# Performance work log

Hardware: AMD Instinct MI355X
Metric: run time of the kernel (lower is better)

Reference implementation:

```python
import jax, jax.numpy as jnp
import numpy as np

DEPTH, HEADS, DIM_HEAD = 6, 8, 64
B, N, E = 2, 128, 160
NUM_ATOMS, NF = 100, 127
DIM = NF + 1                 # 128, node feature dim fed to transformer
INNER = HEADS * DIM_HEAD     # 512


def setup_inputs() -> dict:
    key = jax.random.key(0)
    ks = iter(jax.random.split(key, 40))
    f32 = jnp.float32
    def w(shape, scale=0.02):
        return jax.random.normal(next(ks), shape, dtype=f32) * scale
    inp = {
        "indices": jax.random.randint(next(ks), (B, N), 0, NUM_ATOMS),
        "coordinates": jax.random.normal(next(ks), (B, N, 3), dtype=f32),
        "bonds": jax.random.randint(next(ks), (E, 2), 0, N),
        "noise_level": jax.random.uniform(next(ks), (1,), dtype=f32),
        "atom_emb": w((NUM_ATOMS, NF), 1.0),
        "ln1_g": jnp.ones((DEPTH, DIM), f32), "ln1_b": jnp.zeros((DEPTH, DIM), f32),
        "Wq": w((DEPTH, DIM, INNER)), "bq": jnp.zeros((DEPTH, INNER), f32),
        "Wkv": w((DEPTH, DIM, 2 * INNER)), "bkv": jnp.zeros((DEPTH, 2 * INNER), f32),
        "We": w((DEPTH, 3, INNER)), "be": jnp.zeros((DEPTH, INNER), f32),
        "Wo": w((DEPTH, INNER, DIM)), "bo": jnp.zeros((DEPTH, DIM), f32),
        "Wg1": w((DEPTH, 3 * DIM, 1)),
        "ln2_g": jnp.ones((DEPTH, DIM), f32), "ln2_b": jnp.zeros((DEPTH, DIM), f32),
        "W1": w((DEPTH, DIM, 4 * DIM)), "b1": jnp.zeros((DEPTH, 4 * DIM), f32),
        "W2": w((DEPTH, 4 * DIM, DIM)), "b2": jnp.zeros((DEPTH, DIM), f32),
        "Wg2": w((DEPTH, 3 * DIM, 1)),
        "Wlin": w((DIM, 1)), "blin": jnp.zeros((1,), f32),
    }
    return inp


def _ln(x, g, b, eps=1e-5):
    m = jnp.mean(x, -1, keepdims=True)
    v = jnp.mean((x - m) ** 2, -1, keepdims=True)
    return (x - m) * jax.lax.rsqrt(v + eps) * g + b


def _gated_residual(x, res, Wg):
    # gate = sigmoid(Linear([x, res, x-res])); out = x*gate + res*(1-gate)
    gate = jax.nn.sigmoid(jnp.concatenate([x, res, x - res], -1) @ Wg)  # (B,N,1)
    return x * gate + res * (1.0 - gate)


def _forward(indices, bonds, coordinates, noise_level, atom_emb,
             ln1_g, ln1_b, Wq, bq, Wkv, bkv, We, be, Wo, bo, Wg1,
             ln2_g, ln2_b, W1, b1, W2, b2, Wg2, Wlin, blin):
    b, n = indices.shape
    # nodes_embedding: atom embedding + noise-level channel
    noise = jnp.broadcast_to(noise_level.reshape(1, 1, 1).astype(coordinates.dtype), (b, n, 1))
    nodes = jnp.concatenate([atom_emb[indices], noise], -1)  # (B,N,DIM)
    # edges_embedding: vectorized scatter of per-bond coordinate differences
    i, j = bonds[:, 0], bonds[:, 1]
    diff = coordinates[:, i] - coordinates[:, j]             # (B,E,3)
    edges = jnp.zeros((b, n, n, 3), coordinates.dtype)
    edges = edges.at[:, i, j].set(diff).at[:, j, i].set(-diff)

    scale = DIM_HEAD ** -0.5
    for l in range(DEPTH):
        # PreNorm + edge-biased attention (mask is all-ones -> no-op)
        xn = _ln(nodes, ln1_g[l], ln1_b[l])
        q = (xn @ Wq[l] + bq[l]).reshape(b, n, HEADS, DIM_HEAD)
        k, v = jnp.split(xn @ Wkv[l] + bkv[l], 2, -1)
        k = k.reshape(b, n, HEADS, DIM_HEAD)
        v = v.reshape(b, n, HEADS, DIM_HEAD)
        e = (edges @ We[l] + be[l]).reshape(b, n, n, HEADS, DIM_HEAD)
        kk = k[:, None] + e                                   # (B,i,j,H,D)
        vv = v[:, None] + e
        sim = jnp.einsum('bihd,bijhd->bijh', q, kk) * scale
        attn = jax.nn.softmax(sim, axis=2)                    # softmax over j
        out = jnp.einsum('bijh,bijhd->bihd', attn, vv).reshape(b, n, INNER)
        out = out @ Wo[l] + bo[l]
        nodes = _gated_residual(out, nodes, Wg1[l])
        # PreNorm + FeedForward (exact GELU, mult=4) + gated residual
        xn = _ln(nodes, ln2_g[l], ln2_b[l])
        ff = jax.nn.gelu(xn @ W1[l] + b1[l], approximate=False) @ W2[l] + b2[l]
        nodes = _gated_residual(ff, nodes, Wg2[l])
    return jnp.sum(nodes @ Wlin + blin)


def reference(indices, coordinates, bonds, noise_level, atom_emb,
              ln1_g, ln1_b, Wq, bq, Wkv, bkv, We, be, Wo, bo, Wg1,
              ln2_g, ln2_b, W1, b1, W2, b2, Wg2, Wlin, blin):
    return _forward(indices, bonds, coordinates, noise_level, atom_emb,
                    ln1_g, ln1_b, Wq, bq, Wkv, bkv, We, be, Wo, bo, Wg1,
                    ln2_g, ln2_b, W1, b1, W2, b2, Wg2, Wlin, blin)
```

## Files before the change

### kernel.cpp

```cpp
#include <hip/hip_runtime.h>
#include <hip/hip_fp16.h>
#include <math.h>

#define DEPTH 6
#define NN    128
#define EE    160
#define NF    127
#define DIMM  128
#define INNER 512
#define NNODE 256

typedef _Float16 h2f16 __attribute__((ext_vector_type(2)));

#if defined(__has_builtin)
#if __has_builtin(__builtin_amdgcn_fdot2)
#define HAVE_FDOT2 1
#endif
#endif

__device__ __forceinline__ float fdot2f(h2f16 a, h2f16 b, float c) {
#ifdef HAVE_FDOT2
    return __builtin_amdgcn_fdot2(a, b, c, false);
#else
    return c + (float)a.x * (float)b.x + (float)a.y * (float)b.y;
#endif
}

__device__ __forceinline__ void gload16(const void* g, void* l) {
    __builtin_amdgcn_global_load_lds((const __attribute__((address_space(1))) void*)g,
                                     (__attribute__((address_space(3))) void*)l,
                                     16, 0, 0);
}

template <int N>
__device__ __forceinline__ void wait_vm() {
    __builtin_amdgcn_s_waitcnt((0xF << 8) | (7 << 4) | (N & 0xF) | ((N >> 4) << 14));
}
__device__ __forceinline__ void wait_lgkm0() { __builtin_amdgcn_s_waitcnt(0xC07F); }
__device__ __forceinline__ void sbar0() { __builtin_amdgcn_sched_barrier(0); }

__device__ __forceinline__ void stage16(const char* g, char* lds, int ln) {
#pragma unroll
    for (int i = 0; i < 16; i++)
        gload16(g + i * 1024 + ln * 16, lds + i * 1024);
}


template <int NSTAGE>
__device__ __forceinline__ float gemv512T(const __half* s_xh, const float* wbuf,
                                          const char* nextG, char* wbufc, int ln) {
    const float4* W = (const float4*)((const char*)wbuf + ln * 256);
    const float4* X = (const float4*)s_xh;
    float acc = 0.0f;
    float4 wr[8], xr[8];
#pragma unroll
    for (int i = 0; i < 8; i++) { wr[i] = W[(i + ln) & 15]; xr[i] = X[i]; }
#pragma unroll
    for (int i = 0; i < 8; i++) {
        const h2f16* wh = (const h2f16*)&wr[i];
        const h2f16* xh = (const h2f16*)&xr[i];
        acc = fdot2f(xh[0], wh[0], acc); acc = fdot2f(xh[1], wh[1], acc);
        acc = fdot2f(xh[2], wh[2], acc); acc = fdot2f(xh[3], wh[3], acc);
    }
    float4 wr2[8], xr2[8];
#pragma unroll
    for (int i = 0; i < 8; i++) { wr2[i] = W[(i + 8 + ln) & 15]; xr2[i] = X[i + 8]; }
    if (NSTAGE) {
        sbar0();
        wait_lgkm0();
        sbar0();
        stage16(nextG, wbufc, ln);
    }
#pragma unroll
    for (int i = 0; i < 8; i++) {
        const h2f16* wh = (const h2f16*)&wr2[i];
        const h2f16* xh = (const h2f16*)&xr2[i];
        acc = fdot2f(xh[0], wh[0], acc); acc = fdot2f(xh[1], wh[1], acc);
        acc = fdot2f(xh[2], wh[2], acc); acc = fdot2f(xh[3], wh[3], acc);
    }
    return acc;
}

template <int NSTAGE>
__device__ __forceinline__ float gemv128T(const __half* s_xp, const float* wbuf,
                                          const char* nextG, char* wbufc, int ln) {
    int kq = ln & 3;
    const float4* W = (const float4*)((const char*)wbuf + ln * 256);
    const float4* X = (const float4*)((const char*)s_xp + kq * 272);
    float acc = 0.0f;
    float4 wr[8], xr[8];
#pragma unroll
    for (int i = 0; i < 8; i++) { wr[i] = W[(i + ln) & 15]; xr[i] = X[i]; }
#pragma unroll
    for (int i = 0; i < 8; i++) {
        const h2f16* wh = (const h2f16*)&wr[i];
        const h2f16* xh = (const h2f16*)&xr[i];
        acc = fdot2f(xh[0], wh[0], acc); acc = fdot2f(xh[1], wh[1], acc);
        acc = fdot2f(xh[2], wh[2], acc); acc = fdot2f(xh[3], wh[3], acc);
    }
    float4 wr2[8], xr2[8];
#pragma unroll
    for (int i = 0; i < 8; i++) { wr2[i] = W[(i + 8 + ln) & 15]; xr2[i] = X[i + 8]; }
    if (NSTAGE) {
        sbar0();
        wait_lgkm0();
        sbar0();
        stage16(nextG, wbufc, ln);
    }
#pragma unroll
    for (int i = 0; i < 8; i++) {
        const h2f16* wh = (const h2f16*)&wr2[i];
        const h2f16* xh = (const h2f16*)&xr2[i];
        acc = fdot2f(xh[0], wh[0], acc); acc = fdot2f(xh[1], wh[1], acc);
        acc = fdot2f(xh[2], wh[2], acc); acc = fdot2f(xh[3], wh[3], acc);
    }
    return acc;
}

template <int N>
__device__ __forceinline__ void block_reduce_n(float* vals, float* sbuf) {
#pragma unroll
    for (int off = 32; off > 0; off >>= 1)
#pragma unroll
        for (int q = 0; q < N; q++) vals[q] += __shfl_xor(vals[q], off, 64);
    int wave = threadIdx.x >> 6;
    if ((threadIdx.x & 63) == 0)
#pragma unroll
        for (int q = 0; q < N; q++) sbuf[wave * N + q] = vals[q];
    __syncthreads();
#pragma unroll
    for (int q = 0; q < N; q++) {
        float r = 0.0f;
#pragma unroll
        for (int g = 0; g < 8; g++) r += sbuf[g * N + q];
        vals[q] = r;
    }
    __syncthreads();
}

__device__ __forceinline__ float gelu_exact(float a) {
    return 0.5f * a * (1.0f + erff(a * 0.70710678f));
}

__global__ __launch_bounds__(512) void k_cvt(const float* Wq, const float* Wkv,
                                             const float* Wo, const float* W1,
                                             const float* W2,
                                             __half* hWq, __half* hWkv, __half* hWo,
                                             __half* hW1, __half* hW2,
                                             const float* blin, float* out) {
    if (blockIdx.x == 0 && threadIdx.x == 0) out[0] = 256.0f * blin[0];
    int bid = blockIdx.x;
    int l = bid / 48, rem = bid % 48, mat = rem >> 3, w = rem & 7;
    int t = threadIdx.x;
    const float* src;
    __half* dst;
    int ncols, col0, big;
    if (mat == 0)      { src = Wq  + (size_t)l * 65536;  dst = hWq  + (size_t)l * 65536;          ncols = 512;  col0 = w * 64;       big = 0; }
    else if (mat == 1) { src = Wkv + (size_t)l * 131072; dst = hWkv + (size_t)l * 131072;         ncols = 1024; col0 = w * 64;       big = 0; }
    else if (mat == 2) { src = Wkv + (size_t)l * 131072; dst = hWkv + (size_t)l * 131072 + 65536; ncols = 1024; col0 = 512 + w * 64; big = 0; }
    else if (mat == 3) { src = W1  + (size_t)l * 65536;  dst = hW1  + (size_t)l * 65536;          ncols = 512;  col0 = w * 64;       big = 0; }
    else if (mat == 4) { src = Wo  + (size_t)l * 65536;  dst = hWo  + (size_t)l * 65536;          ncols = 128;  col0 = w * 16;       big = 1; }
    else               { src = W2  + (size_t)l * 65536;  dst = hW2  + (size_t)l * 65536;          ncols = 128;  col0 = w * 16;       big = 1; }
    dst += w * 8192;
#pragma unroll
    for (int p = 0; p < 2; p++) {
        int bi = p * 512 + t;
        int i = bi & 15;
        int ln, c, row0;
        if (!big) { c = bi >> 4; ln = c; row0 = i * 8; }
        else {
            c = bi >> 6;
            int kq = (bi >> 4) & 3;
            ln = c * 4 + kq;
            row0 = kq * 128 + i * 8;
        }
        __align__(16) __half tmp[8];
#pragma unroll
        for (int e = 0; e < 8; e++)
            tmp[e] = __float2half(src[(size_t)(row0 + e) * ncols + col0 + c]);
        *(float4*)&dst[ln * 128 + ((i + ln) & 15) * 8] = *(const float4*)tmp;
    }
}

__global__ __launch_bounds__(512, 1) void k_pre(const int* indices, const float* noise,
                                                const float* atom_emb,
                                                const float* ln1_g, const float* ln1_b,
                                                const __half* hWq, const float* bq,
                                                const __half* hWkv, const float* bkv,
                                                float* nodes, float* qb,
                                                __half* hk, __half* hv) {
    int bn = blockIdx.x;
    int t  = threadIdx.x;
    int d  = t & 127;
    bool own = (t < 128);
    int w = t >> 6, ln = t & 63;
    __shared__ float arena[32768];
    __shared__ __align__(16) __half s_xh[128];
    __shared__ float s_red[48];
    float* wbuf = arena + w * 4096;

    stage16((const char*)hWq + w * 16384, (char*)wbuf, ln);

    float nd = 0.0f;
    if (own) {
        int idx = indices[bn];
        nd = (d < NF) ? atom_emb[idx * NF + d] : noise[0];
        nodes[bn * DIMM + d] = nd;
    }
    float vals[2] = {own ? nd : 0.0f, own ? nd * nd : 0.0f};
    block_reduce_n<2>(vals, s_red);
    float m   = vals[0] * (1.0f / 128.0f);
    float var = vals[1] * (1.0f / 128.0f) - m * m;
    if (own) s_xh[d] = __float2half((nd - m) * rsqrtf(var + 1e-5f) * ln1_g[d] + ln1_b[d]);
    __syncthreads();

    int col = w * 64 + ln;
    wait_vm<0>();
    {
        float q = gemv512T<1>(s_xh, wbuf, (const char*)hWkv + w * 16384, (char*)wbuf, ln);
        qb[(size_t)bn * INNER + col] = q + bq[col];
    }
    wait_vm<0>();
    {
        float k = gemv512T<1>(s_xh, wbuf, (const char*)hWkv + 131072 + w * 16384,
                              (char*)wbuf, ln);
        hk[(size_t)bn * INNER + col] = __float2half(k + bkv[col]);
    }
    wait_vm<0>();
    {
        float v = gemv512T<0>(s_xh, wbuf, nullptr, nullptr, ln);
        hv[(size_t)bn * INNER + col] = __float2half(v + bkv[INNER + col]);
    }
}

__global__ __launch_bounds__(512, 1) void k_layer(int l,
        const float* coords, const int* bonds,
        const float* We, const float* be,
        float* qb, const __half* hkin, const __half* hvin,
        __half* hkout, __half* hvout,
        const __half* hWo, const float* bo, const float* Wg1,
        const float* ln2_g, const float* ln2_b,
        const __half* hW1, const float* b1,
        const __half* hW2, const float* b2,
        const float* Wg2,
        const float* ln1_g, const float* ln1_b,
        const __half* hWq, const float* bq,
        const __half* hWkv, const float* bkv,
        float* nodes, const float* Wlin, float* out) {
    int bn = blockIdx.x;
    int b = bn >> 7, i = bn & 127;
    int t = threadIdx.x;
    int d = t & 127;
    bool own = (t < 128);
    int w = t >> 6, ln = t & 63;

    __shared__ float arena[32768];
    __shared__ float scoord[384];
    __shared__ float sedge[384];
    __shared__ int   sadj[128];
    __shared__ float s_l[64];
    __shared__ __align__(16) __half s_aoh[544];
    __shared__ __align__(16) __half s_hh[544];
    __shared__ __align__(16) __half s_xh[128];
    __shared__ float s_x[128];
    __shared__ float s_red[48];
    __shared__ float s_part[4096];
    float* s_o = s_part;
    float* wbuf = arena + w * 4096;

    const char* WoL  = (const char*)hWo + (size_t)l * 131072 + w * 16384;
    const char* W1L  = (const char*)hW1 + (size_t)l * 131072 + w * 16384;
    const char* W2L  = (const char*)hW2 + (size_t)l * 131072 + w * 16384;
    const char* WqnL = (const char*)hWq + (size_t)(l + 1) * 131072 + w * 16384;
    const char* WknL = (const char*)hWkv + (size_t)(l + 1) * 262144 + w * 16384;
    const char* WvnL = (const char*)hWkv + (size_t)(l + 1) * 262144 + 131072 + w * 16384;

    stage16(WoL, (char*)wbuf, ln);

    const float4* qR4 = (const float4*)(qb + (size_t)bn * INNER);
    const float4* WeR = (const float4*)(We + (size_t)l * 3 * INNER);
    float4 qa  = qR4[ln * 2],        qz  = qR4[ln * 2 + 1];
    float4 w0a = WeR[ln * 2],        w0z = WeR[ln * 2 + 1];
    float4 w1a = WeR[128 + ln * 2],  w1z = WeR[129 + ln * 2];
    float4 w2a = WeR[256 + ln * 2],  w2z = WeR[257 + ln * 2];
    float4 bea = ((const float4*)(be + (size_t)l * INNER))[ln * 2];
    float4 bez = ((const float4*)(be + (size_t)l * INNER))[ln * 2 + 1];
    float res = own ? nodes[bn * DIMM + d] : 0.0f;
    h2f16 qh0 = {(_Float16)qa.x, (_Float16)qa.y};
    h2f16 qh1 = {(_Float16)qa.z, (_Float16)qa.w};
    h2f16 qh2 = {(_Float16)qz.x, (_Float16)qz.y};
    h2f16 qh3 = {(_Float16)qz.z, (_Float16)qz.w};
    float c = qa.x * bea.x + qa.y * bea.y + qa.z * bea.z + qa.w * bea.w
            + qz.x * bez.x + qz.y * bez.y + qz.z * bez.z + qz.w * bez.w;
    c += __shfl_xor(c, 1, 64); c += __shfl_xor(c, 2, 64); c += __shfl_xor(c, 4, 64);

    if (t < 3 * NN) scoord[t] = coords[b * 3 * NN + t];
    if (t < NN) sadj[t] = 0;
    __syncthreads();
    if (t < EE) {
        int e0 = bonds[2 * t], e1 = bonds[2 * t + 1];
        if (e0 == i) sadj[e1] = 1;
        if (e1 == i) sadj[e0] = 1;
    }
    __syncthreads();
    if (t < NN) {
        int j = t;
        float msk = sadj[j] ? 1.0f : 0.0f;
        sedge[3 * j + 0] = msk * (scoord[3 * i + 0] - scoord[3 * j + 0]);
        sedge[3 * j + 1] = msk * (scoord[3 * i + 1] - scoord[3 * j + 1]);
        sedge[3 * j + 2] = msk * (scoord[3 * i + 2] - scoord[3 * j + 2]);
    }
    __syncthreads();

    const float4* kR = (const float4*)(hkin + (size_t)b * NN * INNER);
    const float4* vR = (const float4*)(hvin + (size_t)b * NN * INNER);
    float l_run = 0.0f, S_nb = 0.0f;
    float4 o0 = {0, 0, 0, 0}, o1 = {0, 0, 0, 0};
    int j0 = w * 16;
#pragma unroll
    for (int base = 0; base < 16; base += 4) {
        float4 kraw[4], vraw[4];
#pragma unroll
        for (int p = 0; p < 4; p++) {
            int j = j0 + base + p;
            kraw[p] = kR[j * 64 + ln];
            vraw[p] = vR[j * 64 + ln];
        }
#pragma unroll
        for (int p = 0; p < 4; p++) {
            int j = j0 + base + p;
            const h2f16* kh = (const h2f16*)&kraw[p];
            float s = fdot2f(qh0, kh[0],
                      fdot2f(qh1, kh[1],
                      fdot2f(qh2, kh[2],
                      fdot2f(qh3, kh[3], 0.0f))));
            bool bonded = (sadj[j] != 0);
            float4 e0, e1;
            if (bonded) {
                float ex = sedge[3 * j], ey = sedge[3 * j + 1], ez = sedge[3 * j + 2];
                e0.x = bea.x + ex * w0a.x + ey * w1a.x + ez * w2a.x;
                e0.y = bea.y + ex * w0a.y + ey * w1a.y + ez * w2a.y;
                e0.z = bea.z + ex * w0a.z + ey * w1a.z + ez * w2a.z;
                e0.w = bea.w + ex * w0a.w + ey * w1a.w + ez * w2a.w;
                e1.x = bez.x + ex * w0z.x + ey * w1z.x + ez * w2z.x;
                e1.y = bez.y + ex * w0z.y + ey * w1z.y + ez * w2z.y;
                e1.z = bez.z + ex * w0z.z + ey * w1z.z + ez * w2z.z;
                e1.w = bez.w + ex * w0z.w + ey * w1z.w + ez * w2z.w;
                s += qa.x * e0.x + qa.y * e0.y + qa.z * e0.z + qa.w * e0.w
                   + qz.x * e1.x + qz.y * e1.y + qz.z * e1.z + qz.w * e1.w;
            }
            s += __shfl_xor(s, 1, 64);
            s += __shfl_xor(s, 2, 64);
            s += __shfl_xor(s, 4, 64);
            if (!bonded) s += c;
            float pp = __expf(s * 0.125f);
            l_run += pp;
            const __half2* vh = (const __half2*)&vraw[p];
            float2 v0 = __half22float2(vh[0]), v1 = __half22float2(vh[1]);
            float2 v2 = __half22float2(vh[2]), v3 = __half22float2(vh[3]);
            o0.x += pp * v0.x; o0.y += pp * v0.y; o0.z += pp * v1.x; o0.w += pp * v1.y;
            o1.x += pp * v2.x; o1.y += pp * v2.y; o1.z += pp * v3.x; o1.w += pp * v3.y;
            if (bonded) {
                o0.x += pp * e0.x; o0.y += pp * e0.y; o0.z += pp * e0.z; o0.w += pp * e0.w;
                o1.x += pp * e1.x; o1.y += pp * e1.y; o1.z += pp * e1.z; o1.w += pp * e1.w;
            } else S_nb += pp;
        }
    }
    o0.x += S_nb * bea.x; o0.y += S_nb * bea.y; o0.z += S_nb * bea.z; o0.w += S_nb * bea.w;
    o1.x += S_nb * bez.x; o1.y += S_nb * bez.y; o1.z += S_nb * bez.z; o1.w += S_nb * bez.w;
    ((float4*)(s_o + w * 512))[ln * 2]     = o0;
    ((float4*)(s_o + w * 512))[ln * 2 + 1] = o1;
    if ((ln & 7) == 0) s_l[w * 8 + (ln >> 3)] = l_run;
    __syncthreads();
    {
        float o = 0.0f;
#pragma unroll
        for (int g = 0; g < 8; g++) o += s_o[g * 512 + t];
        int h = t >> 6;
        float lsum = 0.0f;
#pragma unroll
        for (int g = 0; g < 8; g++) lsum += s_l[g * 8 + h];
        s_aoh[(t >> 7) * 136 + (t & 127)] = __float2half(o / lsum);
    }
    __syncthreads();

    wait_vm<0>();
    {
        float xo = gemv128T<1>(s_aoh, wbuf, W1L, (char*)wbuf, ln);
        xo += __shfl_xor(xo, 1, 64);
        xo += __shfl_xor(xo, 2, 64);
        if ((ln & 3) == 0) s_x[w * 16 + (ln >> 2)] = xo;
    }
    __syncthreads();
    float x = own ? s_x[d] + bo[l * DIMM + d] : 0.0f;

    const float* Wg1_l = Wg1 + l * 3 * DIMM;
    float n1;
    {
        float tex = own ? (x * Wg1_l[d] + res * Wg1_l[DIMM + d]
                           + (x - res) * Wg1_l[2 * DIMM + d]) : 0.0f;
        float vals[6] = {tex,
                         own ? x : 0.0f, own ? x * x : 0.0f,
                         own ? x * res : 0.0f,
                         own ? res : 0.0f, own ? res * res : 0.0f};
        block_reduce_n<6>(vals, s_red);
        float g1 = 1.0f / (1.0f + __expf(-vals[0]));
        float sn  = g1 * vals[1] + (1.0f - g1) * vals[4];
        float sn2 = g1 * g1 * vals[2] + 2.0f * g1 * (1.0f - g1) * vals[3]
                  + (1.0f - g1) * (1.0f - g1) * vals[5];
        float m   = sn * (1.0f / 128.0f);
        float var = sn2 * (1.0f / 128.0f) - m * m;
        n1 = x * g1 + res * (1.0f - g1);
        if (own) s_xh[d] = __float2half((n1 - m) * rsqrtf(var + 1e-5f) * ln2_g[l * DIMM + d]
                                        + ln2_b[l * DIMM + d]);
    }
    __syncthreads();

    wait_vm<0>();
    {
        float a1 = gemv512T<1>(s_xh, wbuf, W2L, (char*)wbuf, ln);
        int col = w * 64 + ln;
        float ag = gelu_exact(a1 + b1[l * 4 * DIMM + col]);
        s_hh[(col >> 7) * 136 + (col & 127)] = __float2half(ag);
    }
    __syncthreads();

    wait_vm<0>();
    {
        float yw;
        if (l < DEPTH - 1) yw = gemv128T<1>(s_hh, wbuf, WqnL, (char*)wbuf, ln);
        else               yw = gemv128T<0>(s_hh, wbuf, nullptr, nullptr, ln);
        yw += __shfl_xor(yw, 1, 64);
        yw += __shfl_xor(yw, 2, 64);
        if ((ln & 3) == 0) s_x[w * 16 + (ln >> 2)] = yw;
    }
    __syncthreads();
    float y = own ? s_x[d] + b2[l * DIMM + d] : 0.0f;

    const float* Wg2_l = Wg2 + l * 3 * DIMM;
    if (l < DEPTH - 1) {
        float tex = own ? (y * Wg2_l[d] + n1 * Wg2_l[DIMM + d]
                           + (y - n1) * Wg2_l[2 * DIMM + d]) : 0.0f;
        float vals[6] = {tex,
                         own ? y : 0.0f, own ? y * y : 0.0f,
                         own ? y * n1 : 0.0f,
                         own ? n1 : 0.0f, own ? n1 * n1 : 0.0f};
        block_reduce_n<6>(vals, s_red);
        float g2 = 1.0f / (1.0f + __expf(-vals[0]));
        float sn  = g2 * vals[1] + (1.0f - g2) * vals[4];
        float sn2 = g2 * g2 * vals[2] + 2.0f * g2 * (1.0f - g2) * vals[3]
                  + (1.0f - g2) * (1.0f - g2) * vals[5];
        float m   = sn * (1.0f / 128.0f);
        float var = sn2 * (1.0f / 128.0f) - m * m;
        float n2 = y * g2 + n1 * (1.0f - g2);
        if (own) {
            nodes[bn * DIMM + d] = n2;
            s_xh[d] = __float2half((n2 - m) * rsqrtf(var + 1e-5f) * ln1_g[(l + 1) * DIMM + d]
                                   + ln1_b[(l + 1) * DIMM + d]);
        }
        __syncthreads();

        int col = w * 64 + ln;
        wait_vm<0>();
        {
            float q = gemv512T<1>(s_xh, wbuf, WknL, (char*)wbuf, ln);
            qb[(size_t)bn * INNER + col] = q + bq[(l + 1) * INNER + col];
        }
        wait_vm<0>();
        {
            float kk = gemv512T<1>(s_xh, wbuf, WvnL, (char*)wbuf, ln);
            hkout[(size_t)bn * INNER + col] =
                __float2half(kk + bkv[(l + 1) * 2 * INNER + col]);
        }
        wait_vm<0>();
        {
            float vv = gemv512T<0>(s_xh, wbuf, nullptr, nullptr, ln);
            hvout[(size_t)bn * INNER + col] =
                __float2half(vv + bkv[(l + 1) * 2 * INNER + INNER + col]);
        }
    } else {
        float wl = own ? Wlin[d] : 0.0f;
        float tex = own ? (y * Wg2_l[d] + n1 * Wg2_l[DIMM + d]
                           + (y - n1) * Wg2_l[2 * DIMM + d]) : 0.0f;
        float vals[3] = {tex, y * wl, n1 * wl};
        block_reduce_n<3>(vals, s_red);
        float g2 = 1.0f / (1.0f + __expf(-vals[0]));
        float tot = g2 * vals[1] + (1.0f - g2) * vals[2];
        if (t == 0) atomicAdd(out, tot);
    }
}

extern "C" void kernel_launch(void* const* d_in, const int* in_sizes, int n_in,
                              void* d_out, int out_size, void* d_ws, size_t ws_size,
                              hipStream_t stream) {
    const int*   indices = (const int*)d_in[0];
    const float* coords  = (const float*)d_in[1];
    const int*   bonds   = (const int*)d_in[2];
    const float* noise   = (const float*)d_in[3];
    const float* atom_emb= (const float*)d_in[4];
    const float* ln1_g   = (const float*)d_in[5];
    const float* ln1_b   = (const float*)d_in[6];
    const float* Wq      = (const float*)d_in[7];
    const float* bq      = (const float*)d_in[8];
    const float* Wkv     = (const float*)d_in[9];
    const float* bkv     = (const float*)d_in[10];
    const float* We      = (const float*)d_in[11];
    const float* be      = (const float*)d_in[12];
    const float* Wo      = (const float*)d_in[13];
    const float* bo      = (const float*)d_in[14];
    const float* Wg1     = (const float*)d_in[15];
    const float* ln2_g   = (const float*)d_in[16];
    const float* ln2_b   = (const float*)d_in[17];
    const float* W1      = (const float*)d_in[18];
    const float* b1      = (const float*)d_in[19];
    const float* W2      = (const float*)d_in[20];
    const float* b2      = (const float*)d_in[21];
    const float* Wg2     = (const float*)d_in[22];
    const float* Wlin    = (const float*)d_in[23];
    const float* blin    = (const float*)d_in[24];

    float*  ws    = (float*)d_ws;
    float*  nodes = ws;
    float*  qb    = nodes + NNODE * DIMM;
    __half* hkb   = (__half*)(qb + NNODE * INNER);
    __half* hvb   = hkb + 2 * NNODE * INNER;
    __half* hWq   = hvb + 2 * NNODE * INNER;
    __half* hWkv  = hWq + DEPTH * DIMM * INNER;
    __half* hWo   = hWkv + DEPTH * DIMM * 2 * INNER;
    __half* hW1   = hWo + DEPTH * INNER * DIMM;
    __half* hW2   = hW1 + DEPTH * DIMM * 4 * DIMM;

    k_cvt<<<288, 512, 0, stream>>>(Wq, Wkv, Wo, W1, W2, hWq, hWkv, hWo, hW1, hW2,
                                   blin, (float*)d_out);
    k_pre<<<NNODE, 512, 0, stream>>>(indices, noise, atom_emb, ln1_g, ln1_b,
                                     hWq, bq, hWkv, bkv, nodes, qb, hkb, hvb);
    for (int l = 0; l < DEPTH; l++) {
        const __half* hkin = hkb + (size_t)(l & 1) * NNODE * INNER;
        const __half* hvin = hvb + (size_t)(l & 1) * NNODE * INNER;
        __half* hkout = hkb + (size_t)((l + 1) & 1) * NNODE * INNER;
        __half* hvout = hvb + (size_t)((l + 1) & 1) * NNODE * INNER;
        k_layer<<<NNODE, 512, 0, stream>>>(l, coords, bonds, We, be,
                                           qb, hkin, hvin, hkout, hvout,
                                           hWo, bo, Wg1, ln2_g, ln2_b, hW1, b1, hW2, b2,
                                           Wg2, ln1_g, ln1_b, hWq, bq, hWkv, bkv,
                                           nodes, Wlin, (float*)d_out);
    }
}
```

Before: 245.3 us.

## Merge weight conversion into prelude, precompute edge features, split weight staging into halves

Removes the separate k_cvt launch and folds fp16 weight conversion into k_pre. The layer-0 Q/K/V projections now run directly in fp32 from the raw weights, with a cross-wave partial-sum combine. Edge vectors (masked coordinate differences) are computed once in k_pre and saved to workspace, so each layer kernel reads them instead of rebuilding adjacency. The GEMV helpers change to a new unswizzled layout: they stage weights in two 8 KB halves with partial vmcnt waits, so the next matrix's prefetch overlaps the current compute, and they use four independent accumulators. The trade-off is a heavier prelude with extra syncs, and the bonded test now relies on a nonzero edge vector, which would miss a bond between identical coordinates.

```diff
diff --git a/kernel.cpp b/kernel.cpp
--- a/kernel.cpp
+++ b/kernel.cpp
@@ -39,80 +39,111 @@
 __device__ __forceinline__ void wait_lgkm0() { __builtin_amdgcn_s_waitcnt(0xC07F); }
 __device__ __forceinline__ void sbar0() { __builtin_amdgcn_sched_barrier(0); }
 
-__device__ __forceinline__ void stage16(const char* g, char* lds, int ln) {
-#pragma unroll
-    for (int i = 0; i < 16; i++)
+__device__ __forceinline__ void stage8c(const char* g, char* lds, int ln) {
+#pragma unroll
+    for (int i = 0; i < 8; i++)
         gload16(g + i * 1024 + ln * 16, lds + i * 1024);
 }
-
-
-template <int NSTAGE>
-__device__ __forceinline__ float gemv512T(const __half* s_xh, const float* wbuf,
-                                          const char* nextG, char* wbufc, int ln) {
-    const float4* W = (const float4*)((const char*)wbuf + ln * 256);
+__device__ __forceinline__ void stage8f(const char* g, int rs, char* lds, int ln) {
+#pragma unroll
+    for (int i = 0; i < 8; i++)
+        gload16(g + (size_t)i * rs + ln * 16, lds + i * 1024);
+}
+
+
+template <int NXT>
+__device__ __forceinline__ float gemv512v2(const __half* s_xh, float* wbuf,
+                                           const char* nextG, int ln) {
+    const char* Wb = (const char*)wbuf;
+    float4 wa[8], wb[8];
+    wait_vm<8>();
+#pragma unroll
+    for (int i = 0; i < 8; i++) wa[i] = *(const float4*)(Wb + i * 1024 + ln * 16);
+    sbar0(); wait_lgkm0(); sbar0();
+    if (NXT) { stage8c(nextG, (char*)wbuf, ln); wait_vm<8>(); }
+    else     wait_vm<0>();
+#pragma unroll
+    for (int i = 0; i < 8; i++) wb[i] = *(const float4*)(Wb + 8192 + i * 1024 + ln * 16);
+    sbar0(); wait_lgkm0(); sbar0();
+    if (NXT) stage8c(nextG + 8192, (char*)wbuf + 8192, ln);
     const float4* X = (const float4*)s_xh;
-    float acc = 0.0f;
-    float4 wr[8], xr[8];
-#pragma unroll
-    for (int i = 0; i < 8; i++) { wr[i] = W[(i + ln) & 15]; xr[i] = X[i]; }
+    float a0 = 0, a1 = 0, a2 = 0, a3 = 0;
 #pragma unroll
     for (int i = 0; i < 8; i++) {
-        const h2f16* wh = (const h2f16*)&wr[i];
-        const h2f16* xh = (const h2f16*)&xr[i];
-        acc = fdot2f(xh[0], wh[0], acc); acc = fdot2f(xh[1], wh[1], acc);
-        acc = fdot2f(xh[2], wh[2], acc); acc = fdot2f(xh[3], wh[3], acc);
-    }
-    float4 wr2[8], xr2[8];
-#pragma unroll
-    for (int i = 0; i < 8; i++) { wr2[i] = W[(i + 8 + ln) & 15]; xr2[i] = X[i + 8]; }
-    if (NSTAGE) {
-        sbar0();
-        wait_lgkm0();
-        sbar0();
-        stage16(nextG, wbufc, ln);
+        float4 xv = X[i];
+        const h2f16* wh = (const h2f16*)&wa[i];
+        const h2f16* xh = (const h2f16*)&xv;
+        a0 = fdot2f(xh[0], wh[0], a0); a1 = fdot2f(xh[1], wh[1], a1);
+        a2 = fdot2f(xh[2], wh[2], a2); a3 = fdot2f(xh[3], wh[3], a3);
     }
 #pragma unroll
     for (int i = 0; i < 8; i++) {
-        const h2f16* wh = (const h2f16*)&wr2[i];
-        const h2f16* xh = (const h2f16*)&xr2[i];
-        acc = fdot2f(xh[0], wh[0], acc); acc = fdot2f(xh[1], wh[1], acc);
-        acc = fdot2f(xh[2], wh[2], acc); acc = fdot2f(xh[3], wh[3], acc);
-    }
-    return acc;
-}
-
-template <int NSTAGE>
-__device__ __forceinline__ float gemv128T(const __half* s_xp, const float* wbuf,
-                                          const char* nextG, char* wbufc, int ln) {
-    int kq = ln & 3;
-    const float4* W = (const float4*)((const char*)wbuf + ln * 256);
-    const float4* X = (const float4*)((const char*)s_xp + kq * 272);
-    float acc = 0.0f;
-    float4 wr[8], xr[8];
-#pragma unroll
-    for (int i = 0; i < 8; i++) { wr[i] = W[(i + ln) & 15]; xr[i] = X[i]; }
+        float4 xv = X[8 + i];
+        const h2f16* wh = (const h2f16*)&wb[i];
+        const h2f16* xh = (const h2f16*)&xv;
+        a0 = fdot2f(xh[0], wh[0], a0); a1 = fdot2f(xh[1], wh[1], a1);
+        a2 = fdot2f(xh[2], wh[2], a2); a3 = fdot2f(xh[3], wh[3], a3);
+    }
+    return (a0 + a1) + (a2 + a3);
+}
+
+template <int NXT>
+__device__ __forceinline__ float gemv128v2(const __half* s_xp, float* wbuf,
+                                           const char* nextG, int ln) {
+    const char* Wb = (const char*)wbuf;
+    const char* Xb = (const char*)s_xp + (ln & 3) * 272;
+    float4 wa[8], wb[8];
+    wait_vm<8>();
+#pragma unroll
+    for (int i = 0; i < 8; i++) wa[i] = *(const float4*)(Wb + i * 1024 + ln * 16);
+    sbar0(); wait_lgkm0(); sbar0();
+    if (NXT) { stage8c(nextG, (char*)wbuf, ln); wait_vm<8>(); }
+    else     wait_vm<0>();
+#pragma unroll
+    for (int i = 0; i < 8; i++) wb[i] = *(const float4*)(Wb + 8192 + i * 1024 + ln * 16);
+    sbar0(); wait_lgkm0(); sbar0();
+    if (NXT) stage8c(nextG + 8192, (char*)wbuf + 8192, ln);
+    float a0 = 0, a1 = 0, a2 = 0, a3 = 0;
 #pragma unroll
     for (int i = 0; i < 8; i++) {
-        const h2f16* wh = (const h2f16*)&wr[i];
-        const h2f16* xh = (const h2f16*)&xr[i];
-        acc = fdot2f(xh[0], wh[0], acc); acc = fdot2f(xh[1], wh[1], acc);
-        acc = fdot2f(xh[2], wh[2], acc); acc = fdot2f(xh[3], wh[3], acc);
-    }
-    float4 wr2[8], xr2[8];
-#pragma unroll
-    for (int i = 0; i < 8; i++) { wr2[i] = W[(i + 8 + ln) & 15]; xr2[i] = X[i + 8]; }
-    if (NSTAGE) {
-        sbar0();
-        wait_lgkm0();
-        sbar0();
-        stage16(nextG, wbufc, ln);
+        float4 xv = *(const float4*)(Xb + i * 16);
+        const h2f16* wh = (const h2f16*)&wa[i];
+        const h2f16* xh = (const h2f16*)&xv;
+        a0 = fdot2f(xh[0], wh[0], a0); a1 = fdot2f(xh[1], wh[1], a1);
+        a2 = fdot2f(xh[2], wh[2], a2); a3 = fdot2f(xh[3], wh[3], a3);
     }
 #pragma unroll
     for (int i = 0; i < 8; i++) {
-        const h2f16* wh = (const h2f16*)&wr2[i];
-        const h2f16* xh = (const h2f16*)&xr2[i];
-        acc = fdot2f(xh[0], wh[0], acc); acc = fdot2f(xh[1], wh[1], acc);
-        acc = fdot2f(xh[2], wh[2], acc); acc = fdot2f(xh[3], wh[3], acc);
+        float4 xv = *(const float4*)(Xb + 128 + i * 16);
+        const h2f16* wh = (const h2f16*)&wb[i];
+        const h2f16* xh = (const h2f16*)&xv;
+        a0 = fdot2f(xh[0], wh[0], a0); a1 = fdot2f(xh[1], wh[1], a1);
+        a2 = fdot2f(xh[2], wh[2], a2); a3 = fdot2f(xh[3], wh[3], a3);
+    }
+    return (a0 + a1) + (a2 + a3);
+}
+
+template <int NXT>
+__device__ __forceinline__ float4 gemvf32(const float* s_xn, float* wbuf,
+                                          const char* nextG, int nrs, int w, int ln) {
+    const float4* w4 = (const float4*)wbuf;
+    float4 wr[16];
+    wait_vm<8>();
+#pragma unroll
+    for (int r = 0; r < 8; r++) wr[r] = w4[r * 64 + ln];
+    sbar0(); wait_lgkm0(); sbar0();
+    if (NXT) { stage8f(nextG, nrs, (char*)wbuf, ln); wait_vm<8>(); }
+    else     wait_vm<0>();
+#pragma unroll
+    for (int r = 8; r < 16; r++) wr[r] = w4[r * 64 + ln];
+    sbar0(); wait_lgkm0(); sbar0();
+    if (NXT) stage8f(nextG + (size_t)8 * nrs, nrs, (char*)wbuf + 8192, ln);
+    float4 acc = {0, 0, 0, 0};
+#pragma unroll
+    for (int r = 0; r < 16; r++) {
+        float a = s_xn[w * 16 + r];
+        acc.x += a * wr[r].x; acc.y += a * wr[r].y;
+        acc.z += a * wr[r].z; acc.w += a * wr[r].w;
     }
     return acc;
 }
@@ -142,64 +173,55 @@
     return 0.5f * a * (1.0f + erff(a * 0.70710678f));
 }
 
-__global__ __launch_bounds__(512) void k_cvt(const float* Wq, const float* Wkv,
-                                             const float* Wo, const float* W1,
-                                             const float* W2,
-                                             __half* hWq, __half* hWkv, __half* hWo,
-                                             __half* hW1, __half* hW2,
-                                             const float* blin, float* out) {
-    if (blockIdx.x == 0 && threadIdx.x == 0) out[0] = 256.0f * blin[0];
-    int bid = blockIdx.x;
-    int l = bid / 48, rem = bid % 48, mat = rem >> 3, w = rem & 7;
-    int t = threadIdx.x;
-    const float* src;
-    __half* dst;
-    int ncols, col0, big;
-    if (mat == 0)      { src = Wq  + (size_t)l * 65536;  dst = hWq  + (size_t)l * 65536;          ncols = 512;  col0 = w * 64;       big = 0; }
-    else if (mat == 1) { src = Wkv + (size_t)l * 131072; dst = hWkv + (size_t)l * 131072;         ncols = 1024; col0 = w * 64;       big = 0; }
-    else if (mat == 2) { src = Wkv + (size_t)l * 131072; dst = hWkv + (size_t)l * 131072 + 65536; ncols = 1024; col0 = 512 + w * 64; big = 0; }
-    else if (mat == 3) { src = W1  + (size_t)l * 65536;  dst = hW1  + (size_t)l * 65536;          ncols = 512;  col0 = w * 64;       big = 0; }
-    else if (mat == 4) { src = Wo  + (size_t)l * 65536;  dst = hWo  + (size_t)l * 65536;          ncols = 128;  col0 = w * 16;       big = 1; }
-    else               { src = W2  + (size_t)l * 65536;  dst = hW2  + (size_t)l * 65536;          ncols = 128;  col0 = w * 16;       big = 1; }
-    dst += w * 8192;
-#pragma unroll
-    for (int p = 0; p < 2; p++) {
-        int bi = p * 512 + t;
-        int i = bi & 15;
-        int ln, c, row0;
-        if (!big) { c = bi >> 4; ln = c; row0 = i * 8; }
-        else {
-            c = bi >> 6;
-            int kq = (bi >> 4) & 3;
-            ln = c * 4 + kq;
-            row0 = kq * 128 + i * 8;
-        }
-        __align__(16) __half tmp[8];
-#pragma unroll
-        for (int e = 0; e < 8; e++)
-            tmp[e] = __float2half(src[(size_t)(row0 + e) * ncols + col0 + c]);
-        *(float4*)&dst[ln * 128 + ((i + ln) & 15) * 8] = *(const float4*)tmp;
-    }
-}
-
-__global__ __launch_bounds__(512, 1) void k_pre(const int* indices, const float* noise,
-                                                const float* atom_emb,
-                                                const float* ln1_g, const float* ln1_b,
-                                                const __half* hWq, const float* bq,
-                                                const __half* hWkv, const float* bkv,
-                                                float* nodes, float* qb,
-                                                __half* hk, __half* hv) {
+__global__ __launch_bounds__(512, 1) void k_pre(
+        const int* indices, const float* coords, const int* bonds, const float* noise,
+        const float* atom_emb, const float* ln1_g, const float* ln1_b,
+        const float* Wq, const float* bq, const float* Wkv, const float* bkv,
+        const float* Wo, const float* W1, const float* W2,
+        __half* hWq, __half* hWkv, __half* hWo, __half* hW1, __half* hW2,
+        float* nodes, float* qb, __half* hk, __half* hv, float* sedgews,
+        const float* blin, float* out) {
     int bn = blockIdx.x;
+    int b = bn >> 7, i = bn & 127;
     int t  = threadIdx.x;
     int d  = t & 127;
     bool own = (t < 128);
     int w = t >> 6, ln = t & 63;
     __shared__ float arena[32768];
-    __shared__ __align__(16) __half s_xh[128];
+    __shared__ float scoord[384];
+    __shared__ int   sadj[128];
+    __shared__ float s_xn[128];
     __shared__ float s_red[48];
+    __shared__ float s_part[2048];
     float* wbuf = arena + w * 4096;
-
-    stage16((const char*)hWq + w * 16384, (char*)wbuf, ln);
+    char*  wbufc = (char*)wbuf;
+
+    if (bn == 0 && t == 0) out[0] = 256.0f * blin[0];
+
+    const char* phB[6] = {(const char*)Wq,            (const char*)Wq + 1024,
+                          (const char*)Wkv,           (const char*)Wkv + 1024,
+                          (const char*)Wkv + 2048,    (const char*)Wkv + 3072};
+    const int phRS[6] = {2048, 2048, 4096, 4096, 4096, 4096};
+
+    stage8f(phB[0] + (size_t)(w * 16) * phRS[0], phRS[0], wbufc, ln);
+    stage8f(phB[0] + (size_t)(w * 16 + 8) * phRS[0], phRS[0], wbufc + 8192, ln);
+
+    if (t < 3 * NN) scoord[t] = coords[b * 3 * NN + t];
+    if (t < NN) sadj[t] = 0;
+    __syncthreads();
+    if (t < EE) {
+        int e0 = bonds[2 * t], e1 = bonds[2 * t + 1];
+        if (e0 == i) sadj[e1] = 1;
+        if (e1 == i) sadj[e0] = 1;
+    }
+    __syncthreads();
+    if (t < NN) {
+        int j = t;
+        float msk = sadj[j] ? 1.0f : 0.0f;
+        sedgews[bn * 384 + 3 * j + 0] = msk * (scoord[3 * i + 0] - scoord[3 * j + 0]);
+        sedgews[bn * 384 + 3 * j + 1] = msk * (scoord[3 * i + 1] - scoord[3 * j + 1]);
+        sedgews[bn * 384 + 3 * j + 2] = msk * (scoord[3 * i + 2] - scoord[3 * j + 2]);
+    }
 
     float nd = 0.0f;
     if (own) {
@@ -207,34 +229,80 @@
         nd = (d < NF) ? atom_emb[idx * NF + d] : noise[0];
         nodes[bn * DIMM + d] = nd;
     }
-    float vals[2] = {own ? nd : 0.0f, own ? nd * nd : 0.0f};
-    block_reduce_n<2>(vals, s_red);
-    float m   = vals[0] * (1.0f / 128.0f);
-    float var = vals[1] * (1.0f / 128.0f) - m * m;
-    if (own) s_xh[d] = __float2half((nd - m) * rsqrtf(var + 1e-5f) * ln1_g[d] + ln1_b[d]);
-    __syncthreads();
-
-    int col = w * 64 + ln;
-    wait_vm<0>();
-    {
-        float q = gemv512T<1>(s_xh, wbuf, (const char*)hWkv + w * 16384, (char*)wbuf, ln);
-        qb[(size_t)bn * INNER + col] = q + bq[col];
-    }
-    wait_vm<0>();
-    {
-        float k = gemv512T<1>(s_xh, wbuf, (const char*)hWkv + 131072 + w * 16384,
-                              (char*)wbuf, ln);
-        hk[(size_t)bn * INNER + col] = __float2half(k + bkv[col]);
-    }
-    wait_vm<0>();
-    {
-        float v = gemv512T<0>(s_xh, wbuf, nullptr, nullptr, ln);
-        hv[(size_t)bn * INNER + col] = __float2half(v + bkv[INNER + col]);
-    }
+    {
+        float vals[2] = {own ? nd : 0.0f, own ? nd * nd : 0.0f};
+        block_reduce_n<2>(vals, s_red);
+        float m   = vals[0] * (1.0f / 128.0f);
+        float var = vals[1] * (1.0f / 128.0f) - m * m;
+        if (own) s_xn[d] = (nd - m) * rsqrtf(var + 1e-5f) * ln1_g[d] + ln1_b[d];
+    }
+
+    for (int u = bn * 512 + t; u < 294912; u += NNODE * 512) {
+        int s = u >> 13, within = u & 8191;
+        int l = s / 6, m = s % 6;
+        const float* src; __half* dst; int ncols, colofs, big;
+        if (m == 0)      { src = Wq  + (size_t)l * 65536;  dst = hWq  + (size_t)l * 65536;         ncols = 512;  colofs = 0;   big = 0; }
+        else if (m == 1) { src = Wkv + (size_t)l * 131072; dst = hWkv + (size_t)l * 131072;        ncols = 1024; colofs = 0;   big = 0; }
+        else if (m == 2) { src = Wkv + (size_t)l * 131072; dst = hWkv + (size_t)l * 131072 + 65536;ncols = 1024; colofs = 512; big = 0; }
+        else if (m == 3) { src = W1  + (size_t)l * 65536;  dst = hW1  + (size_t)l * 65536;         ncols = 512;  colofs = 0;   big = 0; }
+        else if (m == 4) { src = Wo  + (size_t)l * 65536;  dst = hWo  + (size_t)l * 65536;         ncols = 128;  colofs = 0;   big = 1; }
+        else             { src = W2  + (size_t)l * 65536;  dst = hW2  + (size_t)l * 65536;         ncols = 128;  colofs = 0;   big = 1; }
+        int rb, col;
+        if (!big) { rb = within >> 9; col = within & 511; }
+        else      { rb = within >> 7; col = within & 127; }
+        int row0 = rb * 8;
+        __align__(16) __half tmp[8];
+#pragma unroll
+        for (int e = 0; e < 8; e++)
+            tmp[e] = __float2half(src[(size_t)(row0 + e) * ncols + colofs + col]);
+        int dh;
+        if (!big) dh = (col >> 6) * 8192 + rb * 512 + (col & 63) * 8;
+        else {
+            int kq = row0 >> 7, ci = (row0 & 127) >> 3;
+            dh = (col >> 4) * 8192 + ci * 512 + ((col & 15) * 4 + kq) * 8;
+        }
+        *(float4*)&dst[dh] = *(const float4*)tmp;
+    }
+    __syncthreads();
+
+#define PRE_COMBINE(P)                                                        \
+    {                                                                         \
+        ((float4*)(s_part + w * 256))[ln] = acc;                              \
+        __syncthreads();                                                      \
+        if (t < 256) {                                                        \
+            float sS = 0.0f;                                                  \
+            _Pragma("unroll")                                                 \
+            for (int g = 0; g < 8; g++) sS += s_part[g * 256 + t];            \
+            int col = ((P) & 1) * 256 + t;                                    \
+            if ((P) < 2)      qb[(size_t)bn * INNER + col] = sS + bq[col];    \
+            else if ((P) < 4) hk[(size_t)bn * INNER + col] =                  \
+                                  __float2half(sS + bkv[col]);                \
+            else              hv[(size_t)bn * INNER + col] =                  \
+                                  __float2half(sS + bkv[INNER + col]);        \
+        }                                                                     \
+        __syncthreads();                                                      \
+    }
+
+    {
+        float4 acc;
+        acc = gemvf32<1>(s_xn, wbuf, phB[1] + (size_t)(w * 16) * phRS[1], phRS[1], w, ln);
+        PRE_COMBINE(0);
+        acc = gemvf32<1>(s_xn, wbuf, phB[2] + (size_t)(w * 16) * phRS[2], phRS[2], w, ln);
+        PRE_COMBINE(1);
+        acc = gemvf32<1>(s_xn, wbuf, phB[3] + (size_t)(w * 16) * phRS[3], phRS[3], w, ln);
+        PRE_COMBINE(2);
+        acc = gemvf32<1>(s_xn, wbuf, phB[4] + (size_t)(w * 16) * phRS[4], phRS[4], w, ln);
+        PRE_COMBINE(3);
+        acc = gemvf32<1>(s_xn, wbuf, phB[5] + (size_t)(w * 16) * phRS[5], phRS[5], w, ln);
+        PRE_COMBINE(4);
+        acc = gemvf32<0>(s_xn, wbuf, nullptr, 0, w, ln);
+        PRE_COMBINE(5);
+    }
+#undef PRE_COMBINE
 }
 
 __global__ __launch_bounds__(512, 1) void k_layer(int l,
-        const float* coords, const int* bonds,
+        const float* sedgews,
         const float* We, const float* be,
         float* qb, const __half* hkin, const __half* hvin,
         __half* hkout, __half* hvout,
@@ -248,16 +316,14 @@
         const __half* hWkv, const float* bkv,
         float* nodes, const float* Wlin, float* out) {
     int bn = blockIdx.x;
-    int b = bn >> 7, i = bn & 127;
+    int b = bn >> 7;
     int t = threadIdx.x;
     int d = t & 127;
     bool own = (t < 128);
     int w = t >> 6, ln = t & 63;
 
     __shared__ float arena[32768];
-    __shared__ float scoord[384];
     __shared__ float sedge[384];
-    __shared__ int   sadj[128];
     __shared__ float s_l[64];
     __shared__ __align__(16) __half s_aoh[544];
     __shared__ __align__(16) __half s_hh[544];
@@ -275,7 +341,8 @@
     const char* WknL = (const char*)hWkv + (size_t)(l + 1) * 262144 + w * 16384;
     const char* WvnL = (const char*)hWkv + (size_t)(l + 1) * 262144 + 131072 + w * 16384;
 
-    stage16(WoL, (char*)wbuf, ln);
+    stage8c(WoL, (char*)wbuf, ln);
+    stage8c(WoL + 8192, (char*)wbuf + 8192, ln);
 
     const float4* qR4 = (const float4*)(qb + (size_t)bn * INNER);
     const float4* WeR = (const float4*)(We + (size_t)l * 3 * INNER);
@@ -294,22 +361,7 @@
             + qz.x * bez.x + qz.y * bez.y + qz.z * bez.z + qz.w * bez.w;
     c += __shfl_xor(c, 1, 64); c += __shfl_xor(c, 2, 64); c += __shfl_xor(c, 4, 64);
 
-    if (t < 3 * NN) scoord[t] = coords[b * 3 * NN + t];
-    if (t < NN) sadj[t] = 0;
-    __syncthreads();
-    if (t < EE) {
-        int e0 = bonds[2 * t], e1 = bonds[2 * t + 1];
-        if (e0 == i) sadj[e1] = 1;
-        if (e1 == i) sadj[e0] = 1;
-    }
-    __syncthreads();
-    if (t < NN) {
-        int j = t;
-        float msk = sadj[j] ? 1.0f : 0.0f;
-        sedge[3 * j + 0] = msk * (scoord[3 * i + 0] - scoord[3 * j + 0]);
-        sedge[3 * j + 1] = msk * (scoord[3 * i + 1] - scoord[3 * j + 1]);
-        sedge[3 * j + 2] = msk * (scoord[3 * i + 2] - scoord[3 * j + 2]);
-    }
+    if (t < 384) sedge[t] = sedgews[bn * 384 + t];
     __syncthreads();
 
     const float4* kR = (const float4*)(hkin + (size_t)b * NN * INNER);
@@ -334,10 +386,10 @@
                       fdot2f(qh1, kh[1],
                       fdot2f(qh2, kh[2],
                       fdot2f(qh3, kh[3], 0.0f))));
-            bool bonded = (sadj[j] != 0);
+            float ex = sedge[3 * j], ey = sedge[3 * j + 1], ez = sedge[3 * j + 2];
+            bool bonded = (ex != 0.0f) || (ey != 0.0f) || (ez != 0.0f);
             float4 e0, e1;
             if (bonded) {
-                float ex = sedge[3 * j], ey = sedge[3 * j + 1], ez = sedge[3 * j + 2];
                 e0.x = bea.x + ex * w0a.x + ey * w1a.x + ez * w2a.x;
                 e0.y = bea.y + ex * w0a.y + ey * w1a.y + ez * w2a.y;
                 e0.z = bea.z + ex * w0a.z + ey * w1a.z + ez * w2a.z;
@@ -384,9 +436,8 @@
     }
     __syncthreads();
 
-    wait_vm<0>();
-    {
-        float xo = gemv128T<1>(s_aoh, wbuf, W1L, (char*)wbuf, ln);
+    {
+        float xo = gemv128v2<1>(s_aoh, wbuf, W1L, ln);
         xo += __shfl_xor(xo, 1, 64);
         xo += __shfl_xor(xo, 2, 64);
         if ((ln & 3) == 0) s_x[w * 16 + (ln >> 2)] = xo;
@@ -416,20 +467,18 @@
     }
     __syncthreads();
 
-    wait_vm<0>();
-    {
-        float a1 = gemv512T<1>(s_xh, wbuf, W2L, (char*)wbuf, ln);
+    {
+        float a1 = gemv512v2<1>(s_xh, wbuf, W2L, ln);
         int col = w * 64 + ln;
         float ag = gelu_exact(a1 + b1[l * 4 * DIMM + col]);
         s_hh[(col >> 7) * 136 + (col & 127)] = __float2half(ag);
     }
     __syncthreads();
 
-    wait_vm<0>();
     {
         float yw;
-        if (l < DEPTH - 1) yw = gemv128T<1>(s_hh, wbuf, WqnL, (char*)wbuf, ln);
-        else               yw = gemv128T<0>(s_hh, wbuf, nullptr, nullptr, ln);
+        if (l < DEPTH - 1) yw = gemv128v2<1>(s_hh, wbuf, WqnL, ln);
+        else               yw = gemv128v2<0>(s_hh, wbuf, nullptr, ln);
         yw += __shfl_xor(yw, 1, 64);
         yw += __shfl_xor(yw, 2, 64);
         if ((ln & 3) == 0) s_x[w * 16 + (ln >> 2)] = yw;
@@ -461,20 +510,17 @@
         __syncthreads();
 
         int col = w * 64 + ln;
-        wait_vm<0>();
         {
-            float q = gemv512T<1>(s_xh, wbuf, WknL, (char*)wbuf, ln);
+            float q = gemv512v2<1>(s_xh, wbuf, WknL, ln);
             qb[(size_t)bn * INNER + col] = q + bq[(l + 1) * INNER + col];
         }
-        wait_vm<0>();
         {
-            float kk = gemv512T<1>(s_xh, wbuf, WvnL, (char*)wbuf, ln);
+            float kk = gemv512v2<1>(s_xh, wbuf, WvnL, ln);
             hkout[(size_t)bn * INNER + col] =
                 __float2half(kk + bkv[(l + 1) * 2 * INNER + col]);
         }
-        wait_vm<0>();
         {
-            float vv = gemv512T<0>(s_xh, wbuf, nullptr, nullptr, ln);
+            float vv = gemv512v2<0>(s_xh, wbuf, nullptr, ln);
             hvout[(size_t)bn * INNER + col] =
                 __float2half(vv + bkv[(l + 1) * 2 * INNER + INNER + col]);
         }
@@ -529,17 +575,18 @@
     __half* hWo   = hWkv + DEPTH * DIMM * 2 * INNER;
     __half* hW1   = hWo + DEPTH * INNER * DIMM;
     __half* hW2   = hW1 + DEPTH * DIMM * 4 * DIMM;
-
-    k_cvt<<<288, 512, 0, stream>>>(Wq, Wkv, Wo, W1, W2, hWq, hWkv, hWo, hW1, hW2,
-                                   blin, (float*)d_out);
-    k_pre<<<NNODE, 512, 0, stream>>>(indices, noise, atom_emb, ln1_g, ln1_b,
-                                     hWq, bq, hWkv, bkv, nodes, qb, hkb, hvb);
+    float*  sedgews = (float*)(hW2 + DEPTH * 4 * DIMM * DIMM);
+
+    k_pre<<<NNODE, 512, 0, stream>>>(indices, coords, bonds, noise, atom_emb,
+                                     ln1_g, ln1_b, Wq, bq, Wkv, bkv, Wo, W1, W2,
+                                     hWq, hWkv, hWo, hW1, hW2,
+                                     nodes, qb, hkb, hvb, sedgews, blin, (float*)d_out);
     for (int l = 0; l < DEPTH; l++) {
         const __half* hkin = hkb + (size_t)(l & 1) * NNODE * INNER;
         const __half* hvin = hvb + (size_t)(l & 1) * NNODE * INNER;
         __half* hkout = hkb + (size_t)((l + 1) & 1) * NNODE * INNER;
         __half* hvout = hvb + (size_t)((l + 1) & 1) * NNODE * INNER;
-        k_layer<<<NNODE, 512, 0, stream>>>(l, coords, bonds, We, be,
+        k_layer<<<NNODE, 512, 0, stream>>>(l, sedgews, We, be,
                                            qb, hkin, hvin, hkout, hvout,
                                            hWo, bo, Wg1, ln2_g, ln2_b, hW1, b1, hW2, b2,
                                            Wg2, ln1_g, ln1_b, hWq, bq, hWkv, bkv,
```

Result: no change. 244.5 us (-0.3%).
